# Kernel optimization log

Measured on AMD Instinct MI355X. Metric: run time of the kernel, lower is better.

## Reference

```python
import jax, jax.numpy as jnp
import numpy as np

EPS_DEFAULT = 1.1920928955078125e-07  # torch fp32 finfo eps used when eps=None


def rms_norm(x, ndims, weight=None, eps=EPS_DEFAULT):
    # normalize over the last `ndims` dims, matching F.rms_norm semantics
    axes = tuple(range(x.ndim - ndims, x.ndim))
    ms = jnp.mean(jnp.square(x), axis=axes, keepdims=True)
    out = x * jax.lax.rsqrt(ms + eps)
    if weight is not None:
        out = out * weight  # weight broadcasts over trailing dims
    return out


def setup_inputs() -> dict:
    key = jax.random.key(0)
    ks = jax.random.split(key, 9)
    B, S = 32, 512
    return {
        "x": jax.random.normal(ks[0], (B, S, 12, 24), dtype=jnp.float32),
        "y": jax.random.normal(ks[1], (B, S, 12, 16), dtype=jnp.float32),
        "z": jax.random.normal(ks[2], (B, S, 12, 16, 24), dtype=jnp.float32),
        "w0": jax.random.uniform(ks[3], (24,), dtype=jnp.float32),
        "w1": jax.random.uniform(ks[4], (12, 16), dtype=jnp.float32),
        "w2": jax.random.uniform(ks[5], (24,), dtype=jnp.float32),
        "w3": jax.random.uniform(ks[6], (24,), dtype=jnp.float32),
        "w4": jax.random.uniform(ks[7], (12, 16), dtype=jnp.float32),
        "w5": jax.random.uniform(ks[8], (24,), dtype=jnp.float32),
    }


def reference(x, y, z, w0, w1, w2, w3, w4, w5):
    # x branch: norm over (24,), then (12,24), then (24,)
    x = rms_norm(x, 1, w0)
    x = rms_norm(x, 2, None)
    x = rms_norm(x, 1, w3)
    # y branch: norm over (16,) eps=1e-3, then (12,16) twice
    y = rms_norm(y, 1, None, eps=0.001)
    y = rms_norm(y, 2, w1)
    y = rms_norm(y, 2, w4)
    # z branch: norm over (24,), then (12,16,24) eps=1e-2, then (24,)
    z = rms_norm(z, 1, w2)
    z = rms_norm(z, 3, None, eps=0.01)
    z = rms_norm(z, 1, w5)
    return (x, y, z)
```

## Files before the change

### kernel.cpp

```cpp
#include <hip/hip_runtime.h>

#define EPS_DEF 1.1920928955078125e-07f


__launch_bounds__(192)
__global__ void fused_rms_kernel(const float* __restrict__ x,
                                 const float* __restrict__ y,
                                 const float* __restrict__ z,
                                 const float* __restrict__ w0,
                                 const float* __restrict__ w1,
                                 const float* __restrict__ w2,
                                 const float* __restrict__ w3,
                                 const float* __restrict__ w4,
                                 const float* __restrict__ w5,
                                 float* __restrict__ ox,
                                 float* __restrict__ oy,
                                 float* __restrict__ oz)
{
    __shared__ __align__(16) float2 part[1152];
    __shared__ float xs[12 * 25];
    __shared__ float ys[12 * 17];
    __shared__ float w0sqs[24], w03s[24];
    __shared__ float w1sqs[192], w14s[192];
    __shared__ float az[192];
    __shared__ float wpart[3][4];

    const int tid = threadIdx.x;
    const int bid = blockIdx.x;
    const int j6  = tid % 6;
    const int c4  = j6 * 4;
    const int r0  = tid / 6;

    float w2v[4], w5v[4];
    #pragma unroll
    for (int k = 0; k < 4; ++k) { w2v[k] = w2[c4 + k]; w5v[k] = w5[c4 + k]; }

    const float4* zp = (const float4*)(z + (size_t)bid * 4608);
    float4 zr[6];
    #pragma unroll
    for (int i = 0; i < 6; ++i) zr[i] = zp[tid + 192 * i];

    if (tid < 72) {
        float4 q = ((const float4*)(x + (size_t)bid * 288))[tid];
        int k = tid * 4, r = k / 24, c = k - r * 24;
        float* d = &xs[r * 25 + c];
        d[0] = q.x; d[1] = q.y; d[2] = q.z; d[3] = q.w;
    } else if (tid < 120) {
        int t = tid - 72;
        float4 q = ((const float4*)(y + (size_t)bid * 192))[t];
        int k = t * 4, r = k / 16, c = k - r * 16;
        float* d = &ys[r * 17 + c];
        d[0] = q.x; d[1] = q.y; d[2] = q.z; d[3] = q.w;
    } else if (tid < 144) {
        int q = tid - 120;
        float a0 = w0[q], a3 = w3[q];
        w0sqs[q] = a0 * a0; w03s[q] = a0 * a3;
    }
    {
        float a1 = w1[tid], a4 = w4[tid];
        w1sqs[tid] = a1 * a1;
        w14s[tid]  = a1 * a4;
    }

    #pragma unroll
    for (int i = 0; i < 6; ++i) {
        float4 q = zr[i];
        float s0 = q.x * q.x;
        s0 = fmaf(q.y, q.y, s0); s0 = fmaf(q.z, q.z, s0); s0 = fmaf(q.w, q.w, s0);
        float t0 = q.x * w2v[0], t1 = q.y * w2v[1], t2 = q.z * w2v[2], t3 = q.w * w2v[3];
        float sw = t0 * t0;
        sw = fmaf(t1, t1, sw); sw = fmaf(t2, t2, sw); sw = fmaf(t3, t3, sw);
        part[tid + 192 * i] = make_float2(s0, sw);
    }
    __syncthreads();

    float s0 = 0.f, swz = 0.f;
    {
        const float4* pr = (const float4*)&part[6 * tid];
        #pragma unroll
        for (int k = 0; k < 3; ++k) {
            float4 p = pr[k];
            s0  += p.x + p.z;
            swz += p.y + p.w;
        }
    }
    const float r1   = rsqrtf(s0 * (1.f / 24.f) + EPS_DEF);
    const float r1sq = r1 * r1;
    float p0 = r1sq * swz, p1 = 0.f, p2 = 0.f, p3 = 0.f;

    float r1x = 0.f, swx = 0.f, r1y = 0.f;
    if (tid < 12) {
        const float* row = &xs[tid * 25];
        float a0 = 0.f, aw = 0.f;
        #pragma unroll
        for (int j = 0; j < 24; ++j) {
            float v = row[j];
            a0 = fmaf(v, v, a0);
            aw = fmaf(v * v, w0sqs[j], aw);
        }
        r1x = rsqrtf(a0 * (1.f / 24.f) + EPS_DEF);
        swx = aw;
        p1  = r1x * r1x * aw;
    } else if (tid < 24) {
        int i = tid - 12;
        const float* row = &ys[i * 17];
        const float* wq  = &w1sqs[i * 16];
        float a0 = 0.f, aw = 0.f;
        #pragma unroll
        for (int j = 0; j < 16; ++j) {
            float v = row[j];
            a0 = fmaf(v, v, a0);
            aw = fmaf(v * v, wq[j], aw);
        }
        r1y = rsqrtf(a0 * (1.f / 16.f) + 1e-3f);
        p2  = r1y * r1y * a0;
        p3  = r1y * r1y * aw;
    }

    #pragma unroll
    for (int d = 32; d; d >>= 1) {
        p0 += __shfl_down(p0, d, 64);
        p1 += __shfl_down(p1, d, 64);
        p2 += __shfl_down(p2, d, 64);
        p3 += __shfl_down(p3, d, 64);
    }
    if ((tid & 63) == 0) {
        int w = tid >> 6;
        wpart[w][0] = p0; wpart[w][1] = p1; wpart[w][2] = p2; wpart[w][3] = p3;
    }
    __syncthreads();

    const float Sz  = wpart[0][0] + wpart[1][0] + wpart[2][0];
    const float Sx  = wpart[0][1] + wpart[1][1] + wpart[2][1];
    const float Sy0 = wpart[0][2] + wpart[1][2] + wpart[2][2];
    const float Sy1 = wpart[0][3] + wpart[1][3] + wpart[2][3];

    const float cZ  = rsqrtf(Sz  * (1.f / 4608.f) + 0.01f);
    const float cX  = rsqrtf(Sx  * (1.f / 288.f)  + EPS_DEF);
    const float c2y = rsqrtf(Sy0 * (1.f / 192.f)  + EPS_DEF);
    const float c3y = rsqrtf(c2y * c2y * Sy1 * (1.f / 192.f) + EPS_DEF);

    {
        float r3 = rsqrtf(cZ * cZ * r1sq * swz * (1.f / 24.f) + EPS_DEF);
        az[tid] = r1 * cZ * r3;
    }
    __syncthreads();

    {
        float w25r[4];
        #pragma unroll
        for (int k = 0; k < 4; ++k) w25r[k] = w2v[k] * w5v[k];
        float4* ozp = (float4*)(oz + (size_t)bid * 4608);
        #pragma unroll
        for (int i = 0; i < 6; ++i) {
            float a = az[r0 + 32 * i];
            float4 q = zr[i];
            q.x *= a * w25r[0];
            q.y *= a * w25r[1];
            q.z *= a * w25r[2];
            q.w *= a * w25r[3];
            ozp[tid + 192 * i] = q;
        }
    }

    if (tid < 12) {
        float r3 = rsqrtf(cX * cX * r1x * r1x * swx * (1.f / 24.f) + EPS_DEF);
        float ax = r1x * cX * r3;
        const float* row = &xs[tid * 25];
        float4* op = (float4*)(ox + (size_t)bid * 288 + tid * 24);
        #pragma unroll
        for (int i = 0; i < 6; ++i) {
            float4 q;
            q.x = row[4*i+0] * ax * w03s[4*i+0];
            q.y = row[4*i+1] * ax * w03s[4*i+1];
            q.z = row[4*i+2] * ax * w03s[4*i+2];
            q.w = row[4*i+3] * ax * w03s[4*i+3];
            op[i] = q;
        }
    } else if (tid < 24) {
        int i = tid - 12;
        float ay = r1y * c2y * c3y;
        const float* row = &ys[i * 17];
        const float* wf  = &w14s[i * 16];
        float4* op = (float4*)(oy + (size_t)bid * 192 + i * 16);
        #pragma unroll
        for (int k = 0; k < 4; ++k) {
            float4 q;
            q.x = row[4*k+0] * ay * wf[4*k+0];
            q.y = row[4*k+1] * ay * wf[4*k+1];
            q.z = row[4*k+2] * ay * wf[4*k+2];
            q.w = row[4*k+3] * ay * wf[4*k+3];
            op[k] = q;
        }
    }
}

extern "C" void kernel_launch(void* const* d_in, const int* in_sizes, int n_in,
                              void* d_out, int out_size, void* d_ws, size_t ws_size,
                              hipStream_t stream) {
    const float* x  = (const float*)d_in[0];
    const float* y  = (const float*)d_in[1];
    const float* z  = (const float*)d_in[2];
    const float* w0 = (const float*)d_in[3];
    const float* w1 = (const float*)d_in[4];
    const float* w2 = (const float*)d_in[5];
    const float* w3 = (const float*)d_in[6];
    const float* w4 = (const float*)d_in[7];
    const float* w5 = (const float*)d_in[8];

    float* out = (float*)d_out;
    const size_t NX = (size_t)32 * 512 * 12 * 24;
    const size_t NY = (size_t)32 * 512 * 12 * 16;
    float* ox = out;
    float* oy = out + NX;
    float* oz = out + NX + NY;

    const int nblk = 32 * 512;
    hipLaunchKernelGGL(fused_rms_kernel, dim3(nblk), dim3(192), 0, stream,
                       x, y, z, w0, w1, w2, w3, w4, w5, ox, oy, oz);
}
```

Baseline: 130.6 us.

## Use nontemporal loads/stores, drop third barrier, spread x/y output across threads

Global loads and stores of x, y and z now use nontemporal builtins on 4-wide vectors. The unpadded x/y shared tiles are copied in directly as vectors. The per-row z scale is no longer precomputed into shared memory behind an extra __syncthreads; each thread recomputes it from stored (r1, sw) pairs. The x/y output is spread over 120 threads with vector stores instead of 24 threads writing whole rows. This removes one barrier and serial store loops, at the cost of redundant rsqrt work and possible LDS bank conflicts from removing the padding.

After: 117.6 us (median of 2 runs). -9.9%, faster.

```diff
diff --git a/kernel.cpp b/kernel.cpp
--- a/kernel.cpp
+++ b/kernel.cpp
@@ -1,6 +1,8 @@
 #include <hip/hip_runtime.h>
 
 #define EPS_DEF 1.1920928955078125e-07f
+
+typedef float f4 __attribute__((ext_vector_type(4)));
 
 
 __launch_bounds__(192)
@@ -18,11 +20,13 @@
                                  float* __restrict__ oz)
 {
     __shared__ __align__(16) float2 part[1152];
-    __shared__ float xs[12 * 25];
-    __shared__ float ys[12 * 17];
-    __shared__ float w0sqs[24], w03s[24];
-    __shared__ float w1sqs[192], w14s[192];
-    __shared__ float az[192];
+    __shared__ __align__(16) float  xs[288];
+    __shared__ __align__(16) float  ys[192];
+    __shared__ float2 rw[192];
+    __shared__ float2 rwx[12];
+    __shared__ float  rwy[12];
+    __shared__ __align__(16) float w0sqs[24], w03s[24];
+    __shared__ __align__(16) float w1sqs[192], w14s[192];
     __shared__ float wpart[3][4];
 
     const int tid = threadIdx.x;
@@ -35,22 +39,19 @@
     #pragma unroll
     for (int k = 0; k < 4; ++k) { w2v[k] = w2[c4 + k]; w5v[k] = w5[c4 + k]; }
 
-    const float4* zp = (const float4*)(z + (size_t)bid * 4608);
-    float4 zr[6];
-    #pragma unroll
-    for (int i = 0; i < 6; ++i) zr[i] = zp[tid + 192 * i];
+    const f4* zp = (const f4*)(z + (size_t)bid * 4608);
+    f4 zr[6];
+    #pragma unroll
+    for (int i = 0; i < 6; ++i)
+        zr[i] = __builtin_nontemporal_load(zp + tid + 192 * i);
 
     if (tid < 72) {
-        float4 q = ((const float4*)(x + (size_t)bid * 288))[tid];
-        int k = tid * 4, r = k / 24, c = k - r * 24;
-        float* d = &xs[r * 25 + c];
-        d[0] = q.x; d[1] = q.y; d[2] = q.z; d[3] = q.w;
+        f4 q = __builtin_nontemporal_load((const f4*)(x + (size_t)bid * 288) + tid);
+        ((f4*)xs)[tid] = q;
     } else if (tid < 120) {
         int t = tid - 72;
-        float4 q = ((const float4*)(y + (size_t)bid * 192))[t];
-        int k = t * 4, r = k / 16, c = k - r * 16;
-        float* d = &ys[r * 17 + c];
-        d[0] = q.x; d[1] = q.y; d[2] = q.z; d[3] = q.w;
+        f4 q = __builtin_nontemporal_load((const f4*)(y + (size_t)bid * 192) + t);
+        ((f4*)ys)[t] = q;
     } else if (tid < 144) {
         int q = tid - 120;
         float a0 = w0[q], a3 = w3[q];
@@ -64,7 +65,7 @@
 
     #pragma unroll
     for (int i = 0; i < 6; ++i) {
-        float4 q = zr[i];
+        f4 q = zr[i];
         float s0 = q.x * q.x;
         s0 = fmaf(q.y, q.y, s0); s0 = fmaf(q.z, q.z, s0); s0 = fmaf(q.w, q.w, s0);
         float t0 = q.x * w2v[0], t1 = q.y * w2v[1], t2 = q.z * w2v[2], t3 = q.w * w2v[3];
@@ -76,21 +77,20 @@
 
     float s0 = 0.f, swz = 0.f;
     {
-        const float4* pr = (const float4*)&part[6 * tid];
+        const f4* pr = (const f4*)&part[6 * tid];
         #pragma unroll
         for (int k = 0; k < 3; ++k) {
-            float4 p = pr[k];
+            f4 p = pr[k];
             s0  += p.x + p.z;
             swz += p.y + p.w;
         }
     }
-    const float r1   = rsqrtf(s0 * (1.f / 24.f) + EPS_DEF);
-    const float r1sq = r1 * r1;
-    float p0 = r1sq * swz, p1 = 0.f, p2 = 0.f, p3 = 0.f;
-
-    float r1x = 0.f, swx = 0.f, r1y = 0.f;
+    const float r1 = rsqrtf(s0 * (1.f / 24.f) + EPS_DEF);
+    rw[tid] = make_float2(r1, swz);
+    float p0 = r1 * r1 * swz, p1 = 0.f, p2 = 0.f, p3 = 0.f;
+
     if (tid < 12) {
-        const float* row = &xs[tid * 25];
+        const float* row = &xs[tid * 24];
         float a0 = 0.f, aw = 0.f;
         #pragma unroll
         for (int j = 0; j < 24; ++j) {
@@ -98,12 +98,12 @@
             a0 = fmaf(v, v, a0);
             aw = fmaf(v * v, w0sqs[j], aw);
         }
-        r1x = rsqrtf(a0 * (1.f / 24.f) + EPS_DEF);
-        swx = aw;
-        p1  = r1x * r1x * aw;
+        float r1x = rsqrtf(a0 * (1.f / 24.f) + EPS_DEF);
+        rwx[tid] = make_float2(r1x, aw);
+        p1 = r1x * r1x * aw;
     } else if (tid < 24) {
         int i = tid - 12;
-        const float* row = &ys[i * 17];
+        const float* row = &ys[i * 16];
         const float* wq  = &w1sqs[i * 16];
         float a0 = 0.f, aw = 0.f;
         #pragma unroll
@@ -112,9 +112,10 @@
             a0 = fmaf(v, v, a0);
             aw = fmaf(v * v, wq[j], aw);
         }
-        r1y = rsqrtf(a0 * (1.f / 16.f) + 1e-3f);
-        p2  = r1y * r1y * a0;
-        p3  = r1y * r1y * aw;
+        float r1y = rsqrtf(a0 * (1.f / 16.f) + 1e-3f);
+        rwy[i] = r1y;
+        p2 = r1y * r1y * a0;
+        p3 = r1y * r1y * aw;
     }
 
     #pragma unroll
@@ -139,59 +140,49 @@
     const float cX  = rsqrtf(Sx  * (1.f / 288.f)  + EPS_DEF);
     const float c2y = rsqrtf(Sy0 * (1.f / 192.f)  + EPS_DEF);
     const float c3y = rsqrtf(c2y * c2y * Sy1 * (1.f / 192.f) + EPS_DEF);
-
-    {
-        float r3 = rsqrtf(cZ * cZ * r1sq * swz * (1.f / 24.f) + EPS_DEF);
-        az[tid] = r1 * cZ * r3;
-    }
-    __syncthreads();
+    const float cZsq = cZ * cZ;
 
     {
         float w25r[4];
         #pragma unroll
         for (int k = 0; k < 4; ++k) w25r[k] = w2v[k] * w5v[k];
-        float4* ozp = (float4*)(oz + (size_t)bid * 4608);
+        f4* ozp = (f4*)(oz + (size_t)bid * 4608);
         #pragma unroll
         for (int i = 0; i < 6; ++i) {
-            float a = az[r0 + 32 * i];
-            float4 q = zr[i];
+            float2 rr = rw[r0 + 32 * i];
+            float r3 = rsqrtf(cZsq * rr.x * rr.x * rr.y * (1.f / 24.f) + EPS_DEF);
+            float a  = rr.x * cZ * r3;
+            f4 q = zr[i];
             q.x *= a * w25r[0];
             q.y *= a * w25r[1];
             q.z *= a * w25r[2];
             q.w *= a * w25r[3];
-            ozp[tid + 192 * i] = q;
-        }
-    }
-
-    if (tid < 12) {
-        float r3 = rsqrtf(cX * cX * r1x * r1x * swx * (1.f / 24.f) + EPS_DEF);
-        float ax = r1x * cX * r3;
-        const float* row = &xs[tid * 25];
-        float4* op = (float4*)(ox + (size_t)bid * 288 + tid * 24);
-        #pragma unroll
-        for (int i = 0; i < 6; ++i) {
-            float4 q;
-            q.x = row[4*i+0] * ax * w03s[4*i+0];
-            q.y = row[4*i+1] * ax * w03s[4*i+1];
-            q.z = row[4*i+2] * ax * w03s[4*i+2];
-            q.w = row[4*i+3] * ax * w03s[4*i+3];
-            op[i] = q;
-        }
-    } else if (tid < 24) {
-        int i = tid - 12;
-        float ay = r1y * c2y * c3y;
-        const float* row = &ys[i * 17];
-        const float* wf  = &w14s[i * 16];
-        float4* op = (float4*)(oy + (size_t)bid * 192 + i * 16);
-        #pragma unroll
-        for (int k = 0; k < 4; ++k) {
-            float4 q;
-            q.x = row[4*k+0] * ay * wf[4*k+0];
-            q.y = row[4*k+1] * ay * wf[4*k+1];
-            q.z = row[4*k+2] * ay * wf[4*k+2];
-            q.w = row[4*k+3] * ay * wf[4*k+3];
-            op[k] = q;
-        }
+            __builtin_nontemporal_store(q, ozp + tid + 192 * i);
+        }
+    }
+
+    if (tid < 72) {
+        int row = tid / 6;
+        float2 rr = rwx[row];
+        float r3 = rsqrtf(cX * cX * rr.x * rr.x * rr.y * (1.f / 24.f) + EPS_DEF);
+        float ax = rr.x * cX * r3;
+        f4 q = ((const f4*)xs)[tid];
+        f4 wf = ((const f4*)w03s)[tid % 6];
+        q.x *= ax * wf.x;
+        q.y *= ax * wf.y;
+        q.z *= ax * wf.z;
+        q.w *= ax * wf.w;
+        __builtin_nontemporal_store(q, (f4*)(ox + (size_t)bid * 288) + tid);
+    } else if (tid < 120) {
+        int t = tid - 72;
+        float ay = rwy[t / 4] * c2y * c3y;
+        f4 q = ((const f4*)ys)[t];
+        f4 wf = ((const f4*)w14s)[t];
+        q.x *= ay * wf.x;
+        q.y *= ay * wf.y;
+        q.z *= ay * wf.z;
+        q.w *= ay * wf.w;
+        __builtin_nontemporal_store(q, (f4*)(oy + (size_t)bid * 192) + t);
     }
 }
 
```
